# Kernel optimization log

Measured on AMD Instinct MI355X. Metric: run time of the kernel, lower is better.

The kernel has to match this reference:

```python
import jax, jax.numpy as jnp
import numpy as np

GRID_SIZE = 64            # scene grid cells at pitch
PITCH = 0.02              # data['resolution']
RES = 0.04                # mast3r_grid_resolution
MAX_PTS = 16              # max_points_in_voxel
MIN_PTS = 15              # min_points_in_voxel
G = int(round(GRID_SIZE * PITCH / RES))   # mast3r grid cells per dim = 32
NUM_VOX = G * G * G                       # 32768
N = 8 * 384 * 512                         # num_images * H * W flattened points


def setup_inputs():
    key = jax.random.key(0)
    k1, k2, k3, k4, k5 = jax.random.split(key, 5)
    half = GRID_SIZE * PITCH / 2 * 1.25   # sample slightly beyond cube -> some out-of-bounds
    pts_0 = jax.random.uniform(k1, (N, 3), jnp.float32, -half, half)
    pts_conf = jax.random.uniform(k2, (N, 1), jnp.float32)
    pts_desc = jax.random.normal(k3, (N, 24), jnp.float32)
    pts_desc_conf = jax.random.uniform(k4, (N, 1), jnp.float32)
    image_ids = jax.random.randint(k5, (N,), 0, 16, jnp.int32)
    center = jnp.zeros((3,), jnp.float32)
    occupancy_grid = jnp.zeros((1, G, G, G), jnp.int32)
    return {"pts_0": pts_0, "pts_conf": pts_conf, "pts_desc": pts_desc,
            "pts_desc_conf": pts_desc_conf, "image_ids": image_ids,
            "center": center, "occupancy_grid": occupancy_grid}


def _voxelize(pts_0, pts_conf, pts_desc, pts_desc_conf, image_ids, center):
    # Hard voxelization with per-voxel point cap, confidence-priority ordering.
    # Fixed-shape (jit-friendly) version: dropped points are masked (zeroed / -1),
    # sentinel bucket NUM_VOX holds out-of-bounds / filtered points.
    n = pts_0.shape[0]
    cube = GRID_SIZE * PITCH
    min_corner = center - cube / 2
    idx = jnp.floor((pts_0 - min_corner) / RES).astype(jnp.int32)
    in_b = jnp.all((idx >= 0) & (idx < G), axis=-1)
    vid = idx[:, 0] * (G * G) + idx[:, 1] * G + idx[:, 2]
    vid = jnp.where(in_b, vid, NUM_VOX)
    ones = jnp.ones((n,), jnp.int32)
    counts0 = jax.ops.segment_sum(ones, vid, num_segments=NUM_VOX + 1)  # bincount
    keep = in_b & (counts0[vid] > MIN_PTS)      # min_points_in_voxel filter
    vid = jnp.where(keep, vid, NUM_VOX)
    # local coords normalized to [-1, 1] within the voxel
    pts_local = (pts_0 - min_corner - idx.astype(pts_0.dtype) * RES - RES / 2) / (RES / 2)
    # stable sort by confidence, descending
    order1 = jnp.argsort(-pts_conf[:, 0], stable=True)
    conf_sorted = pts_conf[order1]
    vid1 = vid[order1]
    # stable sort by voxel id, ascending -> within a voxel, points ordered by conf
    order2 = jnp.argsort(vid1, stable=True)
    vid_sorted = vid1[order2]
    point_sorted = order1[order2]               # indices into original point arrays
    counts = jax.ops.segment_sum(ones, vid_sorted, num_segments=NUM_VOX + 1)
    offsets = jnp.cumsum(counts) - counts
    pos = jnp.arange(n, dtype=jnp.int32) - offsets[vid_sorted].astype(jnp.int32)
    valid = (pos < MAX_PTS) & (vid_sorted < NUM_VOX)   # cap points per voxel
    row = jnp.where(valid, vid_sorted, NUM_VOX)
    col = jnp.clip(pos, 0, MAX_PTS - 1)
    table = jnp.full((NUM_VOX + 1, MAX_PTS), -1, jnp.int32)
    table = table.at[row, col].set(jnp.arange(n, dtype=jnp.int32))[:NUM_VOX]
    vf = valid.astype(pts_0.dtype)
    pts_out = pts_local[point_sorted] * vf[:, None]
    # faithful to source quirk: conf was sorted in place then indexed by point ids
    conf_out = conf_sorted[point_sorted] * vf[:, None]
    desc_out = pts_desc[point_sorted] * vf[:, None]
    desc_conf_out = pts_desc_conf[point_sorted] * vf[:, None]
    img_out = jnp.where(valid, image_ids[point_sorted], -1)
    occupied = (table[:, 0] >= 0).astype(jnp.int32)    # padded analogue of voxel_ids_final
    return pts_out, conf_out, desc_out, desc_conf_out, table, occupied, img_out


def reference(pts_0, pts_conf, pts_desc, pts_desc_conf, image_ids, center, occupancy_grid):
    X = _voxelize(pts_0, pts_conf, pts_desc, pts_desc_conf, image_ids, center)
    return X + (occupancy_grid,)
```

## Files before the change

### kernel.cpp

```cpp
#include <hip/hip_runtime.h>


#define NG 32
#define NVOXEL 32768
#define TILE 4096
#define VCAP 8192
#define CCAP 8192

__device__ __forceinline__ int conf_bucket(float c) {
  int b = (int)(c * 65536.0f);
  return b < 0 ? 0 : (b > 65535 ? 65535 : b);
}

__device__ int block_scan_excl(int v, int* lds) {
  int t = threadIdx.x;
  lds[t] = v;
  __syncthreads();
  for (int off = 1; off < (int)blockDim.x; off <<= 1) {
    int x = (t >= off) ? lds[t - off] : 0;
    __syncthreads();
    lds[t] += x;
    __syncthreads();
  }
  int incl = lds[t];
  __syncthreads();
  return incl - v;
}

__global__ void k_hist(int n, const float* __restrict__ pts, const float* __restrict__ conf,
                       const float* __restrict__ center, unsigned* __restrict__ code,
                       int* __restrict__ blockHistV, int* __restrict__ blockHistC) {
  __shared__ int vh[256], ch[256];
  int t = threadIdx.x;
  vh[t] = 0; ch[t] = 0;
  __syncthreads();
  int base = blockIdx.x * TILE;
  float mx = center[0] - 0.64f, my = center[1] - 0.64f, mz = center[2] - 0.64f;
  for (int r = 0; r < TILE; r += 256) {
    int p = base + r + t;
    if (p < n) {
      float x = pts[3 * p], y = pts[3 * p + 1], z = pts[3 * p + 2];
      int ix = (int)floorf((x - mx) / 0.04f);
      int iy = (int)floorf((y - my) / 0.04f);
      int iz = (int)floorf((z - mz) / 0.04f);
      bool inb = (ix >= 0 && ix < NG && iy >= 0 && iy < NG && iz >= 0 && iz < NG);
      int vid = inb ? (ix * 1024 + iy * 32 + iz) : 0xFFFF;
      int cb = conf_bucket(conf[p]);
      code[p] = ((unsigned)vid << 16) | (unsigned)cb;
      if (inb) atomicAdd(&vh[vid >> 7], 1);
      atomicAdd(&ch[cb >> 8], 1);
    }
  }
  __syncthreads();
  blockHistV[blockIdx.x * 256 + t] = vh[t];
  blockHistC[blockIdx.x * 256 + t] = ch[t];
}

__global__ void k_binprefix(int nblk, const int* __restrict__ blockHistV,
                            const int* __restrict__ blockHistC, int* __restrict__ blockBaseV,
                            int* __restrict__ blockBaseC, int* __restrict__ totals) {
  __shared__ int lds[512];
  int t = threadIdx.x;
  int bin = blockIdx.x & 255;
  int isConf = blockIdx.x >> 8;
  const int* src = isConf ? blockHistC : blockHistV;
  int* dst = isConf ? blockBaseC : blockBaseV;
  int v = (t < nblk) ? src[t * 256 + bin] : 0;
  int ex = block_scan_excl(v, lds);
  if (t < nblk) dst[t * 256 + bin] = ex;
  if (t == nblk - 1) totals[blockIdx.x] = ex + v;
}

__global__ void k_scan_small(const int* __restrict__ totals, int* __restrict__ segStartV,
                             int* __restrict__ segStartC) {
  __shared__ int lds[256];
  int t = threadIdx.x;
  int ev = block_scan_excl(totals[t], lds);
  segStartV[t] = ev;
  __syncthreads();
  int ec = block_scan_excl(totals[256 + t], lds);
  segStartC[t] = ec;
}

__global__ void k_scatter(int n, const unsigned* __restrict__ code, const float* __restrict__ conf,
                          const int* __restrict__ segStartV, const int* __restrict__ segStartC,
                          const int* __restrict__ blockBaseV, const int* __restrict__ blockBaseC,
                          uint2* __restrict__ vidSeg, float* __restrict__ confSeg) {
  __shared__ int curV[256], curC[256];
  int t = threadIdx.x;
  curV[t] = segStartV[t] + blockBaseV[blockIdx.x * 256 + t];
  curC[t] = segStartC[t] + blockBaseC[blockIdx.x * 256 + t];
  __syncthreads();
  int base = blockIdx.x * TILE;
  for (int r = 0; r < TILE; r += 256) {
    int p = base + r + t;
    if (p < n) {
      unsigned u = code[p];
      int cb = (int)(u & 0xFFFFu);
      int vid = (int)(u >> 16);
      float c = conf[p];
      if (vid != 0xFFFF) {
        int loc = atomicAdd(&curV[vid >> 7], 1);
        vidSeg[loc] = make_uint2(((unsigned)p << 7) | (unsigned)(vid & 127),
                                 __float_as_uint(c));
      }
      int loc2 = atomicAdd(&curC[cb >> 8], 1);
      confSeg[loc2] = c;
    }
  }
}

__global__ void k_vox(const uint2* __restrict__ vidSeg, const int* __restrict__ totals,
                      const int* __restrict__ segStartV, uint2* __restrict__ ptlist2,
                      int* __restrict__ counts0, int* __restrict__ rawOff) {
  __shared__ uint2 seg[VCAP];
  __shared__ int vcnt[128], voff[128], scan_t[256];
  int b = blockIdx.x, t = threadIdx.x;
  int s0 = segStartV[b];
  int m = totals[b];
  if (m > VCAP) m = VCAP;
  if (t < 128) vcnt[t] = 0;
  __syncthreads();
  for (int e = t; e < m; e += 256) {
    uint2 pk = vidSeg[s0 + e];
    seg[e] = pk;
    atomicAdd(&vcnt[pk.x & 127u], 1);
  }
  __syncthreads();
  int c = (t < 128) ? vcnt[t] : 0;
  int ex = block_scan_excl(c, scan_t);
  if (t < 128) {
    voff[t] = ex;
    counts0[b * 128 + t] = c;
    rawOff[b * 128 + t] = s0 + ex;
    vcnt[t] = 0;
  }
  __syncthreads();
  for (int e = t; e < m; e += 256) {
    uint2 pk = seg[e];
    int v = (int)(pk.x & 127u);
    int loc = atomicAdd(&vcnt[v], 1);
    ptlist2[s0 + voff[v] + loc] = make_uint2(pk.x >> 7, pk.y);
  }
}

__global__ void k_conf(int n, const float* __restrict__ confSeg, const int* __restrict__ totals,
                       const int* __restrict__ segStartC, float* __restrict__ confSorted) {
  __shared__ float A[CCAP];
  __shared__ float B[CCAP];
  __shared__ int fh[256], foff[257], scan_t[256];
  int b = blockIdx.x, t = threadIdx.x;
  int s0 = segStartC[b];
  int m = totals[256 + b];
  if (m > CCAP) m = CCAP;
  fh[t] = 0;
  __syncthreads();
  for (int e = t; e < m; e += 256) {
    float c = confSeg[s0 + e];
    A[e] = c;
    atomicAdd(&fh[conf_bucket(c) & 255], 1);
  }
  __syncthreads();
  int ex = block_scan_excl(fh[t], scan_t);
  foff[t] = ex;
  if (t == 0) foff[256] = m;
  fh[t] = 0;
  __syncthreads();
  for (int e = t; e < m; e += 256) {
    float c = A[e];
    int f = conf_bucket(c) & 255;
    int loc = atomicAdd(&fh[f], 1);
    B[foff[f] + loc] = c;
  }
  __syncthreads();
  for (int e = t; e < m; e += 256) {
    int lo = 0, hi = 255;
    while (lo < hi) { int mid = (lo + hi + 1) >> 1; if (foff[mid] <= e) lo = mid; else hi = mid - 1; }
    int fend = foff[lo + 1];
    float v = B[e];
    int rank = 0;
    for (int q = foff[lo]; q < fend; q++) {
      float w = B[q];
      rank += (w > v || (w == v && q < e)) ? 1 : 0;
    }
    A[(m - fend) + rank] = v;
  }
  __syncthreads();
  int dstBase = n - (s0 + m);
  for (int e = t; e < m; e += 256) confSorted[dstBase + e] = A[e];
}

__global__ void k_scan_vox(const int* __restrict__ counts0, int* __restrict__ filtOff,
                           int* __restrict__ filtTotal) {
  __shared__ int lds[1024];
  int t = threadIdx.x;
  int base = t * 32;
  int sf = 0;
  for (int k = 0; k < 32; k++) {
    int c = counts0[base + k];
    sf += (c > 15) ? c : 0;
  }
  int ef = block_scan_excl(sf, lds);
  for (int k = 0; k < 32; k++) {
    int c = counts0[base + k];
    filtOff[base + k] = ef;
    ef += (c > 15) ? c : 0;
  }
  if (t == 1023) filtTotal[0] = ef;
}

__global__ void k_select(const int* __restrict__ counts0, const int* __restrict__ rawOff,
                         const int* __restrict__ filtOff, const uint2* __restrict__ ptlist2,
                         int* __restrict__ rowPoint) {
  __shared__ float lc[4 * 256];
  __shared__ int li[4 * 256];
  int wave = threadIdx.x >> 6, lane = threadIdx.x & 63;
  int v = blockIdx.x * 4 + wave;
  int m = counts0[v];
  bool active = (m > 15);
  int base = rawOff[v];
  int staged = m < 256 ? m : 256;
  float* LC = &lc[wave * 256];
  int* LI = &li[wave * 256];
  if (active) {
    for (int e = lane; e < staged; e += 64) {
      uint2 pk = ptlist2[base + e];
      LI[e] = (int)pk.x;
      LC[e] = __uint_as_float(pk.y);
    }
  }
  __syncthreads();
  if (active) {
    int out0 = filtOff[v];
    for (int e = lane; e < m; e += 64) {
      int pe; float ce;
      if (e < staged) { pe = LI[e]; ce = LC[e]; }
      else { uint2 pk = ptlist2[base + e]; pe = (int)pk.x; ce = __uint_as_float(pk.y); }
      int rank = 0;
      for (int q = 0; q < m; q++) {
        float cq; int pq;
        if (q < staged) { cq = LC[q]; pq = LI[q]; }
        else { uint2 pk = ptlist2[base + q]; pq = (int)pk.x; cq = __uint_as_float(pk.y); }
        rank += (cq > ce || (cq == ce && pq < pe)) ? 1 : 0;
      }
      rowPoint[out0 + rank] = (rank < 16) ? pe : -1;
    }
  }
}

__global__ void k_emit(int n, const int* __restrict__ rowPoint, const int* __restrict__ filtTotal,
                       const float* __restrict__ pts, const float* __restrict__ confSorted,
                       const float* __restrict__ dconf, const int* __restrict__ imgid,
                       const float4* __restrict__ desc, const float* __restrict__ center,
                       const int* __restrict__ counts0, const int* __restrict__ filtOff,
                       const int* __restrict__ occ_in, float* __restrict__ pts_out,
                       float* __restrict__ conf_out, float4* __restrict__ desc_out,
                       float* __restrict__ dconf_out, float* __restrict__ table_out,
                       float* __restrict__ occupied_out, float* __restrict__ img_out,
                       float* __restrict__ occgrid_out) {
  int j = blockIdx.x * blockDim.x + threadIdx.x;
  int T = filtTotal[0];
  if (j < 6 * n) {
    int i = j / 6, c = j - 6 * i;
    int p = (i < T) ? rowPoint[i] : -1;
    float4 val = make_float4(0.f, 0.f, 0.f, 0.f);
    if (p >= 0) val = desc[p * 6 + c];
    desc_out[j] = val;
    return;
  }
  int j2 = j - 6 * n;
  if (j2 < 3 * n) {
    int i = j2 / 3, c = j2 - 3 * i;
    int p = (i < T) ? rowPoint[i] : -1;
    float o = 0.0f;
    if (p >= 0) {
      float mc = center[c] - 0.64f;
      float x = pts[3 * p + c];
      float fx = floorf((x - mc) / 0.04f);
      o = (x - mc - fx * 0.04f - 0.02f) / 0.02f;
    }
    pts_out[j2] = o;
    return;
  }
  j2 -= 3 * n;
  if (j2 < n) {
    int p = (j2 < T) ? rowPoint[j2] : -1;
    conf_out[j2] = (p >= 0) ? confSorted[p] : 0.0f;
    return;
  }
  j2 -= n;
  if (j2 < n) {
    int p = (j2 < T) ? rowPoint[j2] : -1;
    dconf_out[j2] = (p >= 0) ? dconf[p] : 0.0f;
    return;
  }
  j2 -= n;
  if (j2 < n) {
    int p = (j2 < T) ? rowPoint[j2] : -1;
    img_out[j2] = (p >= 0) ? (float)imgid[p] : -1.0f;
    return;
  }
  j2 -= n;
  if (j2 < NVOXEL * 16) {
    int v = j2 >> 4, c = j2 & 15;
    bool occ = counts0[v] > 15;
    table_out[j2] = occ ? (float)(filtOff[v] + c) : -1.0f;
    return;
  }
  j2 -= NVOXEL * 16;
  if (j2 < NVOXEL) {
    occupied_out[j2] = (counts0[j2] > 15) ? 1.0f : 0.0f;
    return;
  }
  j2 -= NVOXEL;
  if (j2 < NVOXEL) occgrid_out[j2] = (float)occ_in[j2];
}

extern "C" void kernel_launch(void* const* d_in, const int* in_sizes, int n_in,
                              void* d_out, int out_size, void* d_ws, size_t ws_size,
                              hipStream_t stream) {
  const int N = in_sizes[0] / 3;
  const float* pts   = (const float*)d_in[0];
  const float* conf  = (const float*)d_in[1];
  const float* desc  = (const float*)d_in[2];
  const float* dconf = (const float*)d_in[3];
  const int* imgid   = (const int*)d_in[4];
  const float* center = (const float*)d_in[5];
  const int* occg    = (const int*)d_in[6];

  float* out = (float*)d_out;
  float* pts_out      = out;
  float* conf_out     = out + (size_t)3 * N;
  float* desc_out     = out + (size_t)4 * N;
  float* dconf_out    = out + (size_t)28 * N;
  float* table_out    = out + (size_t)29 * N;
  float* occupied_out = table_out + (size_t)NVOXEL * 16;
  float* img_out      = occupied_out + NVOXEL;
  float* occgrid_out  = img_out + N;

  const int nTiles = (N + TILE - 1) / TILE;

  char* w = (char*)d_ws;
  unsigned* code   = (unsigned*)w; w += (size_t)N * 4;
  uint2* vidSeg    = (uint2*)w;    w += (size_t)N * 8;
  float* confSeg   = (float*)w;    w += (size_t)N * 4;
  float* confSort  = (float*)w;    w += (size_t)N * 4;
  uint2* ptlist2   = (uint2*)w;    w += (size_t)N * 8;
  int* rowPoint    = (int*)w;      w += (size_t)N * 4;
  int* counts0     = (int*)w;      w += (size_t)NVOXEL * 4;
  int* rawOff      = (int*)w;      w += (size_t)NVOXEL * 4;
  int* filtOff     = (int*)w;      w += (size_t)NVOXEL * 4;
  int* blockHistV  = (int*)w;      w += (size_t)nTiles * 256 * 4;
  int* blockHistC  = (int*)w;      w += (size_t)nTiles * 256 * 4;
  int* blockBaseV  = (int*)w;      w += (size_t)nTiles * 256 * 4;
  int* blockBaseC  = (int*)w;      w += (size_t)nTiles * 256 * 4;
  int* totals      = (int*)w;      w += 512 * 4;
  int* segStartV   = (int*)w;      w += 256 * 4;
  int* segStartC   = (int*)w;      w += 256 * 4;
  int* filtTotal   = (int*)w;      w += 4;

  const int B = 256;

  k_hist<<<nTiles, B, 0, stream>>>(N, pts, conf, center, code, blockHistV, blockHistC);
  k_binprefix<<<512, 512, 0, stream>>>(nTiles, blockHistV, blockHistC, blockBaseV, blockBaseC,
                                       totals);
  k_scan_small<<<1, 256, 0, stream>>>(totals, segStartV, segStartC);
  k_scatter<<<nTiles, B, 0, stream>>>(N, code, conf, segStartV, segStartC, blockBaseV,
                                      blockBaseC, vidSeg, confSeg);
  k_vox<<<256, 256, 0, stream>>>(vidSeg, totals, segStartV, ptlist2, counts0, rawOff);
  k_conf<<<256, 256, 0, stream>>>(N, confSeg, totals, segStartC, confSort);
  k_scan_vox<<<1, 1024, 0, stream>>>(counts0, filtOff, filtTotal);
  k_select<<<NVOXEL / 4, 256, 0, stream>>>(counts0, rawOff, filtOff, ptlist2, rowPoint);

  const long long totalJ = 12LL * N + (long long)NVOXEL * 16 + 2LL * NVOXEL;
  const int gE = (int)((totalJ + B - 1) / B);
  k_emit<<<gE, B, 0, stream>>>(N, rowPoint, filtTotal, pts, confSort, dconf, imgid,
                               (const float4*)desc, center, counts0, filtOff, occg, pts_out,
                               conf_out, (float4*)desc_out, dconf_out, table_out, occupied_out,
                               img_out, occgrid_out);
}
```

Before: 227.9 us.

## Fuse scan into scatter, merge voxel and conf sort kernels, shrink code buffer

Removes the separate single-block segment-start scan kernel by recomputing the 256-entry scan redundantly in every scatter and sort block. The voxel-bucketing and confidence-sort kernels become one 512-block launch that shares LDS, so both independent passes can run concurrently. The per-point code buffer shrinks to 16 bits, with the confidence bucket recomputed in scatter, which cuts intermediate traffic. Emit stores become nontemporal. This trades two fewer launches and less memory traffic for redundant per-block scans.

```diff
diff --git a/kernel.cpp b/kernel.cpp
--- a/kernel.cpp
+++ b/kernel.cpp
@@ -7,6 +7,8 @@
 #define VCAP 8192
 #define CCAP 8192
 
+typedef float v4f __attribute__((ext_vector_type(4)));
+
 __device__ __forceinline__ int conf_bucket(float c) {
   int b = (int)(c * 65536.0f);
   return b < 0 ? 0 : (b > 65535 ? 65535 : b);
@@ -27,9 +29,12 @@
   return incl - v;
 }
 
-__global__ void k_hist(int n, const float* __restrict__ pts, const float* __restrict__ conf,
-                       const float* __restrict__ center, unsigned* __restrict__ code,
-                       int* __restrict__ blockHistV, int* __restrict__ blockHistC) {
+__global__ __launch_bounds__(256) void k_hist(int n, const float* __restrict__ pts,
+                                              const float* __restrict__ conf,
+                                              const float* __restrict__ center,
+                                              unsigned short* __restrict__ code,
+                                              int* __restrict__ blockHistV,
+                                              int* __restrict__ blockHistC) {
   __shared__ int vh[256], ch[256];
   int t = threadIdx.x;
   vh[t] = 0; ch[t] = 0;
@@ -45,10 +50,9 @@
       int iz = (int)floorf((z - mz) / 0.04f);
       bool inb = (ix >= 0 && ix < NG && iy >= 0 && iy < NG && iz >= 0 && iz < NG);
       int vid = inb ? (ix * 1024 + iy * 32 + iz) : 0xFFFF;
-      int cb = conf_bucket(conf[p]);
-      code[p] = ((unsigned)vid << 16) | (unsigned)cb;
+      code[p] = (unsigned short)vid;
       if (inb) atomicAdd(&vh[vid >> 7], 1);
-      atomicAdd(&ch[cb >> 8], 1);
+      atomicAdd(&ch[conf_bucket(conf[p]) >> 8], 1);
     }
   }
   __syncthreads();
@@ -71,34 +75,27 @@
   if (t == nblk - 1) totals[blockIdx.x] = ex + v;
 }
 
-__global__ void k_scan_small(const int* __restrict__ totals, int* __restrict__ segStartV,
-                             int* __restrict__ segStartC) {
-  __shared__ int lds[256];
-  int t = threadIdx.x;
-  int ev = block_scan_excl(totals[t], lds);
-  segStartV[t] = ev;
-  __syncthreads();
-  int ec = block_scan_excl(totals[256 + t], lds);
-  segStartC[t] = ec;
-}
-
-__global__ void k_scatter(int n, const unsigned* __restrict__ code, const float* __restrict__ conf,
-                          const int* __restrict__ segStartV, const int* __restrict__ segStartC,
-                          const int* __restrict__ blockBaseV, const int* __restrict__ blockBaseC,
-                          uint2* __restrict__ vidSeg, float* __restrict__ confSeg) {
-  __shared__ int curV[256], curC[256];
-  int t = threadIdx.x;
-  curV[t] = segStartV[t] + blockBaseV[blockIdx.x * 256 + t];
-  curC[t] = segStartC[t] + blockBaseC[blockIdx.x * 256 + t];
+__global__ __launch_bounds__(256) void k_scatter(int n, const unsigned short* __restrict__ code,
+                                                 const float* __restrict__ conf,
+                                                 const int* __restrict__ totals,
+                                                 const int* __restrict__ blockBaseV,
+                                                 const int* __restrict__ blockBaseC,
+                                                 uint2* __restrict__ vidSeg,
+                                                 float* __restrict__ confSeg) {
+  __shared__ int curV[256], curC[256], lds[256];
+  int t = threadIdx.x;
+  int exV = block_scan_excl(totals[t], lds);
+  int exC = block_scan_excl(totals[256 + t], lds);
+  curV[t] = exV + blockBaseV[blockIdx.x * 256 + t];
+  curC[t] = exC + blockBaseC[blockIdx.x * 256 + t];
   __syncthreads();
   int base = blockIdx.x * TILE;
   for (int r = 0; r < TILE; r += 256) {
     int p = base + r + t;
     if (p < n) {
-      unsigned u = code[p];
-      int cb = (int)(u & 0xFFFFu);
-      int vid = (int)(u >> 16);
+      int vid = code[p];
       float c = conf[p];
+      int cb = conf_bucket(c);
       if (vid != 0xFFFF) {
         int loc = atomicAdd(&curV[vid >> 7], 1);
         vidSeg[loc] = make_uint2(((unsigned)p << 7) | (unsigned)(vid & 127),
@@ -110,84 +107,92 @@
   }
 }
 
-__global__ void k_vox(const uint2* __restrict__ vidSeg, const int* __restrict__ totals,
-                      const int* __restrict__ segStartV, uint2* __restrict__ ptlist2,
-                      int* __restrict__ counts0, int* __restrict__ rawOff) {
+__global__ __launch_bounds__(256) void k_voxconf(int n, const uint2* __restrict__ vidSeg,
+                                                 const float* __restrict__ confSeg,
+                                                 const int* __restrict__ totals,
+                                                 uint2* __restrict__ ptlist2,
+                                                 int* __restrict__ counts0,
+                                                 int* __restrict__ rawOff,
+                                                 float* __restrict__ confSorted) {
   __shared__ uint2 seg[VCAP];
-  __shared__ int vcnt[128], voff[128], scan_t[256];
-  int b = blockIdx.x, t = threadIdx.x;
-  int s0 = segStartV[b];
-  int m = totals[b];
-  if (m > VCAP) m = VCAP;
-  if (t < 128) vcnt[t] = 0;
-  __syncthreads();
-  for (int e = t; e < m; e += 256) {
-    uint2 pk = vidSeg[s0 + e];
-    seg[e] = pk;
-    atomicAdd(&vcnt[pk.x & 127u], 1);
-  }
-  __syncthreads();
-  int c = (t < 128) ? vcnt[t] : 0;
-  int ex = block_scan_excl(c, scan_t);
-  if (t < 128) {
-    voff[t] = ex;
-    counts0[b * 128 + t] = c;
-    rawOff[b * 128 + t] = s0 + ex;
-    vcnt[t] = 0;
-  }
-  __syncthreads();
-  for (int e = t; e < m; e += 256) {
-    uint2 pk = seg[e];
-    int v = (int)(pk.x & 127u);
-    int loc = atomicAdd(&vcnt[v], 1);
-    ptlist2[s0 + voff[v] + loc] = make_uint2(pk.x >> 7, pk.y);
-  }
-}
-
-__global__ void k_conf(int n, const float* __restrict__ confSeg, const int* __restrict__ totals,
-                       const int* __restrict__ segStartC, float* __restrict__ confSorted) {
-  __shared__ float A[CCAP];
-  __shared__ float B[CCAP];
-  __shared__ int fh[256], foff[257], scan_t[256];
-  int b = blockIdx.x, t = threadIdx.x;
-  int s0 = segStartC[b];
-  int m = totals[256 + b];
-  if (m > CCAP) m = CCAP;
-  fh[t] = 0;
-  __syncthreads();
-  for (int e = t; e < m; e += 256) {
-    float c = confSeg[s0 + e];
-    A[e] = c;
-    atomicAdd(&fh[conf_bucket(c) & 255], 1);
-  }
-  __syncthreads();
-  int ex = block_scan_excl(fh[t], scan_t);
-  foff[t] = ex;
-  if (t == 0) foff[256] = m;
-  fh[t] = 0;
-  __syncthreads();
-  for (int e = t; e < m; e += 256) {
-    float c = A[e];
-    int f = conf_bucket(c) & 255;
-    int loc = atomicAdd(&fh[f], 1);
-    B[foff[f] + loc] = c;
-  }
-  __syncthreads();
-  for (int e = t; e < m; e += 256) {
-    int lo = 0, hi = 255;
-    while (lo < hi) { int mid = (lo + hi + 1) >> 1; if (foff[mid] <= e) lo = mid; else hi = mid - 1; }
-    int fend = foff[lo + 1];
-    float v = B[e];
-    int rank = 0;
-    for (int q = foff[lo]; q < fend; q++) {
-      float w = B[q];
-      rank += (w > v || (w == v && q < e)) ? 1 : 0;
-    }
-    A[(m - fend) + rank] = v;
-  }
-  __syncthreads();
-  int dstBase = n - (s0 + m);
-  for (int e = t; e < m; e += 256) confSorted[dstBase + e] = A[e];
+  __shared__ int cnt[257], off2[257], scan_t[256];
+  __shared__ int s0_sh;
+  int t = threadIdx.x;
+  if (blockIdx.x < 256) {
+    int b = blockIdx.x;
+    int ex = block_scan_excl(totals[t], scan_t);
+    if (t == b) s0_sh = ex;
+    if (t < 128) cnt[t] = 0;
+    __syncthreads();
+    int s0 = s0_sh;
+    int m = totals[b];
+    if (m > VCAP) m = VCAP;
+    for (int e = t; e < m; e += 256) {
+      uint2 pk = vidSeg[s0 + e];
+      seg[e] = pk;
+      atomicAdd(&cnt[pk.x & 127u], 1);
+    }
+    __syncthreads();
+    int c = (t < 128) ? cnt[t] : 0;
+    int ex2 = block_scan_excl(c, scan_t);
+    if (t < 128) {
+      off2[t] = ex2;
+      counts0[b * 128 + t] = c;
+      rawOff[b * 128 + t] = s0 + ex2;
+      cnt[t] = 0;
+    }
+    __syncthreads();
+    for (int e = t; e < m; e += 256) {
+      uint2 pk = seg[e];
+      int v = (int)(pk.x & 127u);
+      int loc = atomicAdd(&cnt[v], 1);
+      ptlist2[s0 + off2[v] + loc] = make_uint2(pk.x >> 7, pk.y);
+    }
+  } else {
+    int b = blockIdx.x - 256;
+    float* A = (float*)seg;
+    float* B = A + CCAP;
+    int ex = block_scan_excl(totals[256 + t], scan_t);
+    if (t == b) s0_sh = ex;
+    cnt[t] = 0;
+    __syncthreads();
+    int s0 = s0_sh;
+    int m = totals[256 + b];
+    if (m > CCAP) m = CCAP;
+    for (int e = t; e < m; e += 256) {
+      float c = confSeg[s0 + e];
+      A[e] = c;
+      atomicAdd(&cnt[conf_bucket(c) & 255], 1);
+    }
+    __syncthreads();
+    int ex2 = block_scan_excl(cnt[t], scan_t);
+    off2[t] = ex2;
+    if (t == 0) off2[256] = m;
+    cnt[t] = 0;
+    __syncthreads();
+    for (int e = t; e < m; e += 256) {
+      float c = A[e];
+      int f = conf_bucket(c) & 255;
+      int loc = atomicAdd(&cnt[f], 1);
+      B[off2[f] + loc] = c;
+    }
+    __syncthreads();
+    for (int e = t; e < m; e += 256) {
+      int lo = 0, hi = 255;
+      while (lo < hi) { int mid = (lo + hi + 1) >> 1; if (off2[mid] <= e) lo = mid; else hi = mid - 1; }
+      int fend = off2[lo + 1];
+      float v = B[e];
+      int rank = 0;
+      for (int q = off2[lo]; q < fend; q++) {
+        float w = B[q];
+        rank += (w > v || (w == v && q < e)) ? 1 : 0;
+      }
+      A[(m - fend) + rank] = v;
+    }
+    __syncthreads();
+    int dstBase = n - (s0 + m);
+    for (int e = t; e < m; e += 256) confSorted[dstBase + e] = A[e];
+  }
 }
 
 __global__ void k_scan_vox(const int* __restrict__ counts0, int* __restrict__ filtOff,
@@ -209,9 +214,11 @@
   if (t == 1023) filtTotal[0] = ef;
 }
 
-__global__ void k_select(const int* __restrict__ counts0, const int* __restrict__ rawOff,
-                         const int* __restrict__ filtOff, const uint2* __restrict__ ptlist2,
-                         int* __restrict__ rowPoint) {
+__global__ __launch_bounds__(256) void k_select(const int* __restrict__ counts0,
+                                                const int* __restrict__ rawOff,
+                                                const int* __restrict__ filtOff,
+                                                const uint2* __restrict__ ptlist2,
+                                                int* __restrict__ rowPoint) {
   __shared__ float lc[4 * 256];
   __shared__ int li[4 * 256];
   int wave = threadIdx.x >> 6, lane = threadIdx.x & 63;
@@ -248,24 +255,25 @@
   }
 }
 
-__global__ void k_emit(int n, const int* __restrict__ rowPoint, const int* __restrict__ filtTotal,
-                       const float* __restrict__ pts, const float* __restrict__ confSorted,
-                       const float* __restrict__ dconf, const int* __restrict__ imgid,
-                       const float4* __restrict__ desc, const float* __restrict__ center,
-                       const int* __restrict__ counts0, const int* __restrict__ filtOff,
-                       const int* __restrict__ occ_in, float* __restrict__ pts_out,
-                       float* __restrict__ conf_out, float4* __restrict__ desc_out,
-                       float* __restrict__ dconf_out, float* __restrict__ table_out,
-                       float* __restrict__ occupied_out, float* __restrict__ img_out,
-                       float* __restrict__ occgrid_out) {
+__global__ __launch_bounds__(256) void k_emit(
+    int n, const int* __restrict__ rowPoint, const int* __restrict__ filtTotal,
+    const float* __restrict__ pts, const float* __restrict__ confSorted,
+    const float* __restrict__ dconf, const int* __restrict__ imgid,
+    const v4f* __restrict__ desc, const float* __restrict__ center,
+    const int* __restrict__ counts0, const int* __restrict__ filtOff,
+    const int* __restrict__ occ_in, float* __restrict__ pts_out,
+    float* __restrict__ conf_out, v4f* __restrict__ desc_out,
+    float* __restrict__ dconf_out, float* __restrict__ table_out,
+    float* __restrict__ occupied_out, float* __restrict__ img_out,
+    float* __restrict__ occgrid_out) {
   int j = blockIdx.x * blockDim.x + threadIdx.x;
   int T = filtTotal[0];
   if (j < 6 * n) {
     int i = j / 6, c = j - 6 * i;
     int p = (i < T) ? rowPoint[i] : -1;
-    float4 val = make_float4(0.f, 0.f, 0.f, 0.f);
+    v4f val = {0.f, 0.f, 0.f, 0.f};
     if (p >= 0) val = desc[p * 6 + c];
-    desc_out[j] = val;
+    __builtin_nontemporal_store(val, &desc_out[j]);
     return;
   }
   int j2 = j - 6 * n;
@@ -279,41 +287,49 @@
       float fx = floorf((x - mc) / 0.04f);
       o = (x - mc - fx * 0.04f - 0.02f) / 0.02f;
     }
-    pts_out[j2] = o;
+    __builtin_nontemporal_store(o, &pts_out[j2]);
     return;
   }
   j2 -= 3 * n;
   if (j2 < n) {
     int p = (j2 < T) ? rowPoint[j2] : -1;
-    conf_out[j2] = (p >= 0) ? confSorted[p] : 0.0f;
+    float o = (p >= 0) ? confSorted[p] : 0.0f;
+    __builtin_nontemporal_store(o, &conf_out[j2]);
     return;
   }
   j2 -= n;
   if (j2 < n) {
     int p = (j2 < T) ? rowPoint[j2] : -1;
-    dconf_out[j2] = (p >= 0) ? dconf[p] : 0.0f;
+    float o = (p >= 0) ? dconf[p] : 0.0f;
+    __builtin_nontemporal_store(o, &dconf_out[j2]);
     return;
   }
   j2 -= n;
   if (j2 < n) {
     int p = (j2 < T) ? rowPoint[j2] : -1;
-    img_out[j2] = (p >= 0) ? (float)imgid[p] : -1.0f;
+    float o = (p >= 0) ? (float)imgid[p] : -1.0f;
+    __builtin_nontemporal_store(o, &img_out[j2]);
     return;
   }
   j2 -= n;
   if (j2 < NVOXEL * 16) {
     int v = j2 >> 4, c = j2 & 15;
     bool occ = counts0[v] > 15;
-    table_out[j2] = occ ? (float)(filtOff[v] + c) : -1.0f;
+    float o = occ ? (float)(filtOff[v] + c) : -1.0f;
+    __builtin_nontemporal_store(o, &table_out[j2]);
     return;
   }
   j2 -= NVOXEL * 16;
   if (j2 < NVOXEL) {
-    occupied_out[j2] = (counts0[j2] > 15) ? 1.0f : 0.0f;
+    float o = (counts0[j2] > 15) ? 1.0f : 0.0f;
+    __builtin_nontemporal_store(o, &occupied_out[j2]);
     return;
   }
   j2 -= NVOXEL;
-  if (j2 < NVOXEL) occgrid_out[j2] = (float)occ_in[j2];
+  if (j2 < NVOXEL) {
+    float o = (float)occ_in[j2];
+    __builtin_nontemporal_store(o, &occgrid_out[j2]);
+  }
 }
 
 extern "C" void kernel_launch(void* const* d_in, const int* in_sizes, int n_in,
@@ -341,12 +357,13 @@
   const int nTiles = (N + TILE - 1) / TILE;
 
   char* w = (char*)d_ws;
-  unsigned* code   = (unsigned*)w; w += (size_t)N * 4;
   uint2* vidSeg    = (uint2*)w;    w += (size_t)N * 8;
+  uint2* ptlist2   = (uint2*)w;    w += (size_t)N * 8;
   float* confSeg   = (float*)w;    w += (size_t)N * 4;
   float* confSort  = (float*)w;    w += (size_t)N * 4;
-  uint2* ptlist2   = (uint2*)w;    w += (size_t)N * 8;
   int* rowPoint    = (int*)w;      w += (size_t)N * 4;
+  unsigned short* code = (unsigned short*)w; w += (size_t)N * 2;
+  w = (char*)(((size_t)w + 255) & ~(size_t)255);
   int* counts0     = (int*)w;      w += (size_t)NVOXEL * 4;
   int* rawOff      = (int*)w;      w += (size_t)NVOXEL * 4;
   int* filtOff     = (int*)w;      w += (size_t)NVOXEL * 4;
@@ -355,8 +372,6 @@
   int* blockBaseV  = (int*)w;      w += (size_t)nTiles * 256 * 4;
   int* blockBaseC  = (int*)w;      w += (size_t)nTiles * 256 * 4;
   int* totals      = (int*)w;      w += 512 * 4;
-  int* segStartV   = (int*)w;      w += 256 * 4;
-  int* segStartC   = (int*)w;      w += 256 * 4;
   int* filtTotal   = (int*)w;      w += 4;
 
   const int B = 256;
@@ -364,18 +379,17 @@
   k_hist<<<nTiles, B, 0, stream>>>(N, pts, conf, center, code, blockHistV, blockHistC);
   k_binprefix<<<512, 512, 0, stream>>>(nTiles, blockHistV, blockHistC, blockBaseV, blockBaseC,
                                        totals);
-  k_scan_small<<<1, 256, 0, stream>>>(totals, segStartV, segStartC);
-  k_scatter<<<nTiles, B, 0, stream>>>(N, code, conf, segStartV, segStartC, blockBaseV,
-                                      blockBaseC, vidSeg, confSeg);
-  k_vox<<<256, 256, 0, stream>>>(vidSeg, totals, segStartV, ptlist2, counts0, rawOff);
-  k_conf<<<256, 256, 0, stream>>>(N, confSeg, totals, segStartC, confSort);
+  k_scatter<<<nTiles, B, 0, stream>>>(N, code, conf, totals, blockBaseV, blockBaseC,
+                                      vidSeg, confSeg);
+  k_voxconf<<<512, B, 0, stream>>>(N, vidSeg, confSeg, totals, ptlist2, counts0, rawOff,
+                                   confSort);
   k_scan_vox<<<1, 1024, 0, stream>>>(counts0, filtOff, filtTotal);
   k_select<<<NVOXEL / 4, 256, 0, stream>>>(counts0, rawOff, filtOff, ptlist2, rowPoint);
 
   const long long totalJ = 12LL * N + (long long)NVOXEL * 16 + 2LL * NVOXEL;
   const int gE = (int)((totalJ + B - 1) / B);
   k_emit<<<gE, B, 0, stream>>>(N, rowPoint, filtTotal, pts, confSort, dconf, imgid,
-                               (const float4*)desc, center, counts0, filtOff, occg, pts_out,
-                               conf_out, (float4*)desc_out, dconf_out, table_out, occupied_out,
+                               (const v4f*)desc, center, counts0, filtOff, occg, pts_out,
+                               conf_out, (v4f*)desc_out, dconf_out, table_out, occupied_out,
                                img_out, occgrid_out);
 }
```

New measurement: 209.9 us. -7.9%, faster.
